# Kernel optimization log

Hardware: AMD Instinct MI355X
Metric: run time of the kernel (lower is better)

## Reference

```python
import jax, jax.numpy as jnp
import numpy as np


def setup_inputs() -> dict:
    key = jax.random.key(0)
    k1, k2, k3 = jax.random.split(key, 3)
    B, H, S, D = 4, 16, 2048, 64
    queries = jax.random.normal(k1, (B, H, S, D), dtype=jnp.float32)
    keys = jax.random.normal(k2, (B, H, S, D), dtype=jnp.float32)
    values = jax.random.normal(k3, (B, H, S, D), dtype=jnp.float32)
    return {"queries": queries, "keys": keys, "values": values, "d_k": D}


def reference(queries, keys, values, d_k):
    # scores = Q K^T / sqrt(d_k)  -> [B, H, S, S]
    scale = 1.0 / jnp.sqrt(jnp.asarray(d_k, dtype=queries.dtype))
    scores = jnp.einsum("bhqd,bhkd->bhqk", queries, keys) * scale
    weights = jax.nn.softmax(scores, axis=-1)
    # out = weights V -> [B, H, S, D]
    return jnp.einsum("bhqk,bhkd->bhqd", weights, values)
```

## Files before the change

kernel.cpp:

```cpp
#include <hip/hip_runtime.h>
#include <hip/hip_bf16.h>

typedef __attribute__((ext_vector_type(8))) short short8;
typedef __attribute__((ext_vector_type(4))) short short4v;
typedef __attribute__((ext_vector_type(16))) float f32x16;

constexpr int Sn = 2048, Dn = 64;
constexpr int KVB = 64;
constexpr int QB  = 256;
constexpr int NT  = Sn / KVB;
constexpr int KSTR = 72;
constexpr int VSTR = 68;
constexpr float QSC = 0.18033688011112042f;

struct SMemS { short K[2][KVB][KSTR]; short Vt[2][Dn][VSTR]; };
union  SMem  { SMemS s; float ep[4][32][36]; };

__device__ inline unsigned cvt_pk_bf16(float a, float b) {
  unsigned r;
  asm("v_cvt_pk_bf16_f32 %0, %1, %2" : "=v"(r) : "v"(a), "v"(b));
  return r;
}
__device__ inline short8 catw(unsigned a, unsigned b, unsigned c, unsigned d) {
  union { unsigned u[4]; short8 s; } t;
  t.u[0]=a; t.u[1]=b; t.u[2]=c; t.u[3]=d;
  return t.s;
}
__device__ inline short8 pack8(float4 a, float4 b) {
  return catw(cvt_pk_bf16(a.x,a.y), cvt_pk_bf16(a.z,a.w),
              cvt_pk_bf16(b.x,b.y), cvt_pk_bf16(b.z,b.w));
}
__device__ inline short8 cat4(short4v a, short4v b) {
  short8 r;
  r[0]=a[0]; r[1]=a[1]; r[2]=a[2]; r[3]=a[3];
  r[4]=b[0]; r[5]=b[1]; r[6]=b[2]; r[7]=b[3];
  return r;
}

__global__ __launch_bounds__(256, 2)
void attn_fwd(const float* __restrict__ Qm, const float* __restrict__ Km,
              const float* __restrict__ Vm, float* __restrict__ Om) {
  __shared__ alignas(16) SMem sm;

  const int fid = blockIdx.x + (blockIdx.y << 3);
  const int xcd = fid & 7, w = fid >> 3;
  const int qt = w & 7, bh = (xcd << 3) | (w >> 3);

  const size_t base = (size_t)bh * Sn * Dn;
  const float* Qb = Qm + base;
  const float* Kb = Km + base;
  const float* Vb = Vm + base;
  float*       Ob = Om + base;

  const int tid = threadIdx.x, wv = tid >> 6, lane = tid & 63;
  const int il = lane & 31, hi = lane >> 5;
  const int qr0 = qt * QB + wv * 64;

  short8 qf[2][4];
#pragma unroll
  for (int u = 0; u < 2; ++u)
#pragma unroll
    for (int ks = 0; ks < 4; ++ks) {
      const float4* qp = (const float4*)(Qb + (size_t)(qr0 + u*32 + il) * Dn + ks*16 + hi*8);
      float4 a = qp[0], b = qp[1];
      a.x*=QSC; a.y*=QSC; a.z*=QSC; a.w*=QSC;
      b.x*=QSC; b.y*=QSC; b.z*=QSC; b.w*=QSC;
      qf[u][ks] = pack8(a, b);
    }

  f32x16 acc[2][2];
#pragma unroll
  for (int u = 0; u < 2; ++u)
#pragma unroll
    for (int dt = 0; dt < 2; ++dt)
#pragma unroll
      for (int r = 0; r < 16; ++r) acc[u][dt][r] = 0.f;
  float lacc[2][8];
#pragma unroll
  for (int u = 0; u < 2; ++u)
#pragma unroll
    for (int r = 0; r < 8; ++r) lacc[u][r] = 0.f;

  f32x16 fz;
#pragma unroll
  for (int r = 0; r < 16; ++r) fz[r] = 0.f;

  const int krow = tid >> 2, kc = (tid & 3) * 16;
  const int vd = tid & 63, vk0 = (tid >> 6) * 8;

  auto stageK = [&](int buf, float4 a0, float4 a1, float4 a2, float4 a3) {
    *(short8*)&sm.s.K[buf][krow][kc]     = pack8(a0, a1);
    *(short8*)&sm.s.K[buf][krow][kc + 8] = pack8(a2, a3);
  };
  auto stageV = [&](int buf, const float* vv) {
#pragma unroll
    for (int c = 0; c < 2; ++c) {
      union { unsigned u[2]; short4v s; } t0, t1;
      t0.u[0] = cvt_pk_bf16(vv[c*8+0], vv[c*8+1]);
      t0.u[1] = cvt_pk_bf16(vv[c*8+2], vv[c*8+3]);
      t1.u[0] = cvt_pk_bf16(vv[c*8+4], vv[c*8+5]);
      t1.u[1] = cvt_pk_bf16(vv[c*8+6], vv[c*8+7]);
      short* p = &sm.s.Vt[buf][vd][vk0 + c*32];
      *(short4v*)p       = t0.s;
      *(short4v*)(p + 4) = t1.s;
    }
  };

  {
    const float4* kp = (const float4*)(Kb + (size_t)krow * Dn + kc);
    float4 a0 = kp[0], a1 = kp[1], a2 = kp[2], a3 = kp[3];
    float vv[16];
#pragma unroll
    for (int c = 0; c < 2; ++c)
#pragma unroll
      for (int j = 0; j < 8; ++j) vv[c*8+j] = Vb[(size_t)(vk0 + c*32 + j) * Dn + vd];
    stageK(0, a0, a1, a2, a3);
    stageV(0, vv);
  }
  __syncthreads();

  int cur = 0;
  for (int t = 0; t < NT; ++t) {
    const bool pf = (t + 1 < NT);
    float4 na0, na1, na2, na3; float nv[16];
    if (pf) {
      const int kvn = (t + 1) * KVB;
      const float4* kp = (const float4*)(Kb + (size_t)(kvn + krow) * Dn + kc);
      na0 = kp[0]; na1 = kp[1]; na2 = kp[2]; na3 = kp[3];
#pragma unroll
      for (int c = 0; c < 2; ++c)
#pragma unroll
        for (int j = 0; j < 8; ++j) nv[c*8+j] = Vb[(size_t)(kvn + vk0 + c*32 + j) * Dn + vd];
    }

    short8 kf[2][4];
#pragma unroll
    for (int h = 0; h < 2; ++h)
#pragma unroll
      for (int ks = 0; ks < 4; ++ks)
        kf[h][ks] = *(const short8*)&sm.s.K[cur][h*32 + il][ks*16 + hi*8];

    short8 vr[8];
#pragma unroll
    for (int h = 0; h < 2; ++h)
#pragma unroll
      for (int dt = 0; dt < 2; ++dt) {
        const short* vrow = &sm.s.Vt[cur][dt*32 + il][h*32];
        vr[h*4+dt*2+0] = cat4(*(const short4v*)(vrow + 4*hi),      *(const short4v*)(vrow + 8  + 4*hi));
        vr[h*4+dt*2+1] = cat4(*(const short4v*)(vrow + 16 + 4*hi), *(const short4v*)(vrow + 24 + 4*hi));
      }

    f32x16 sa[2][2];
#pragma unroll
    for (int u = 0; u < 2; ++u)
#pragma unroll
      for (int h = 0; h < 2; ++h) {
        sa[u][h] = __builtin_amdgcn_mfma_f32_32x32x16_bf16(kf[h][0], qf[u][0], fz, 0, 0, 0);
#pragma unroll
        for (int ks = 1; ks < 4; ++ks)
          sa[u][h] = __builtin_amdgcn_mfma_f32_32x32x16_bf16(kf[h][ks], qf[u][ks], sa[u][h], 0, 0, 0);
      }

    short8 pb[2][2][2];
#pragma unroll
    for (int u = 0; u < 2; ++u) {
#pragma unroll
      for (int h = 0; h < 2; ++h)
#pragma unroll
        for (int r = 0; r < 16; ++r) sa[u][h][r] = __builtin_amdgcn_exp2f(sa[u][h][r]);
      float ta[16];
#pragma unroll
      for (int r = 0; r < 16; ++r) ta[r] = sa[u][0][r] + sa[u][1][r];
#pragma unroll
      for (int r = 0; r < 8; ++r) lacc[u][r] += ta[r] + ta[r + 8];

#pragma unroll
      for (int h = 0; h < 2; ++h) {
        pb[u][h][0] = catw(cvt_pk_bf16(sa[u][h][0],  sa[u][h][1]),  cvt_pk_bf16(sa[u][h][2],  sa[u][h][3]),
                           cvt_pk_bf16(sa[u][h][4],  sa[u][h][5]),  cvt_pk_bf16(sa[u][h][6],  sa[u][h][7]));
        pb[u][h][1] = catw(cvt_pk_bf16(sa[u][h][8],  sa[u][h][9]),  cvt_pk_bf16(sa[u][h][10], sa[u][h][11]),
                           cvt_pk_bf16(sa[u][h][12], sa[u][h][13]), cvt_pk_bf16(sa[u][h][14], sa[u][h][15]));
      }
    }

    if (pf) { stageK(cur ^ 1, na0, na1, na2, na3); stageV(cur ^ 1, nv); }

#pragma unroll
    for (int h = 0; h < 2; ++h)
#pragma unroll
      for (int dt = 0; dt < 2; ++dt)
#pragma unroll
        for (int u = 0; u < 2; ++u) {
          acc[u][dt] = __builtin_amdgcn_mfma_f32_32x32x16_bf16(vr[h*4+dt*2+0], pb[u][h][0], acc[u][dt], 0, 0, 0);
          acc[u][dt] = __builtin_amdgcn_mfma_f32_32x32x16_bf16(vr[h*4+dt*2+1], pb[u][h][1], acc[u][dt], 0, 0, 0);
        }
    __syncthreads();
    cur ^= 1;
  }

  const int q2 = lane >> 1, dh = (lane & 1) * 16;
#pragma unroll
  for (int u = 0; u < 2; ++u) {
    float l0 = (lacc[u][0] + lacc[u][4]) + (lacc[u][1] + lacc[u][5]);
    float l1 = (lacc[u][2] + lacc[u][6]) + (lacc[u][3] + lacc[u][7]);
    float l  = l0 + l1;
    l += __shfl_xor(l, 32);
    const float inv = 1.0f / l;
#pragma unroll
    for (int dt = 0; dt < 2; ++dt) {
#pragma unroll
      for (int r = 0; r < 16; ++r) {
        int dcol = (r & 3) + 8 * (r >> 2) + 4 * hi;
        sm.ep[wv][il][dcol] = acc[u][dt][r] * inv;
      }
#pragma unroll
      for (int i = 0; i < 4; ++i) {
        float4 o = *(const float4*)&sm.ep[wv][q2][dh + i*4];
        *(float4*)(Ob + (size_t)(qr0 + u*32 + q2) * Dn + dt*32 + dh + i*4) = o;
      }
    }
  }
}

extern "C" void kernel_launch(void* const* d_in, const int* in_sizes, int n_in,
                              void* d_out, int out_size, void* d_ws, size_t ws_size,
                              hipStream_t stream) {
  const float* Q = (const float*)d_in[0];
  const float* K = (const float*)d_in[1];
  const float* V = (const float*)d_in[2];
  float* O = (float*)d_out;
  dim3 grid(Sn / QB, 4 * 16);
  attn_fwd<<<grid, 256, 0, stream>>>(Q, K, V, O);
}
```

Measured before the change: 85.71 us.

## Process two 64-row KV sub-tiles per barrier to halve synchronisation count

```diff
diff --git a/kernel.cpp b/kernel.cpp
--- a/kernel.cpp
+++ b/kernel.cpp
@@ -6,14 +6,13 @@
 typedef __attribute__((ext_vector_type(16))) float f32x16;
 
 constexpr int Sn = 2048, Dn = 64;
-constexpr int KVB = 64;
 constexpr int QB  = 256;
-constexpr int NT  = Sn / KVB;
+constexpr int NI  = Sn / 128;
 constexpr int KSTR = 72;
 constexpr int VSTR = 68;
 constexpr float QSC = 0.18033688011112042f;
 
-struct SMemS { short K[2][KVB][KSTR]; short Vt[2][Dn][VSTR]; };
+struct SMemS { short K[2][2][64][KSTR]; short Vt[2][2][64][VSTR]; };
 union  SMem  { SMemS s; float ep[4][32][36]; };
 
 __device__ inline unsigned cvt_pk_bf16(float a, float b) {
@@ -88,11 +87,22 @@
   const int krow = tid >> 2, kc = (tid & 3) * 16;
   const int vd = tid & 63, vk0 = (tid >> 6) * 8;
 
-  auto stageK = [&](int buf, float4 a0, float4 a1, float4 a2, float4 a3) {
-    *(short8*)&sm.s.K[buf][krow][kc]     = pack8(a0, a1);
-    *(short8*)&sm.s.K[buf][krow][kc + 8] = pack8(a2, a3);
-  };
-  auto stageV = [&](int buf, const float* vv) {
+  auto loadK = [&](int kvbase, float4* ka) {
+    const float4* kp = (const float4*)(Kb + (size_t)(kvbase + krow) * Dn + kc);
+#pragma unroll
+    for (int i = 0; i < 4; ++i) ka[i] = kp[i];
+  };
+  auto loadV = [&](int kvbase, float* vv) {
+#pragma unroll
+    for (int c = 0; c < 2; ++c)
+#pragma unroll
+      for (int j = 0; j < 8; ++j) vv[c*8+j] = Vb[(size_t)(kvbase + vk0 + c*32 + j) * Dn + vd];
+  };
+  auto stageK = [&](int buf, int sub, const float4* ka) {
+    *(short8*)&sm.s.K[buf][sub][krow][kc]     = pack8(ka[0], ka[1]);
+    *(short8*)&sm.s.K[buf][sub][krow][kc + 8] = pack8(ka[2], ka[3]);
+  };
+  auto stageV = [&](int buf, int sub, const float* vv) {
 #pragma unroll
     for (int c = 0; c < 2; ++c) {
       union { unsigned u[2]; short4v s; } t0, t1;
@@ -100,52 +110,26 @@
       t0.u[1] = cvt_pk_bf16(vv[c*8+2], vv[c*8+3]);
       t1.u[0] = cvt_pk_bf16(vv[c*8+4], vv[c*8+5]);
       t1.u[1] = cvt_pk_bf16(vv[c*8+6], vv[c*8+7]);
-      short* p = &sm.s.Vt[buf][vd][vk0 + c*32];
+      short* p = &sm.s.Vt[buf][sub][vd][vk0 + c*32];
       *(short4v*)p       = t0.s;
       *(short4v*)(p + 4) = t1.s;
     }
   };
 
-  {
-    const float4* kp = (const float4*)(Kb + (size_t)krow * Dn + kc);
-    float4 a0 = kp[0], a1 = kp[1], a2 = kp[2], a3 = kp[3];
-    float vv[16];
-#pragma unroll
-    for (int c = 0; c < 2; ++c)
-#pragma unroll
-      for (int j = 0; j < 8; ++j) vv[c*8+j] = Vb[(size_t)(vk0 + c*32 + j) * Dn + vd];
-    stageK(0, a0, a1, a2, a3);
-    stageV(0, vv);
-  }
-  __syncthreads();
-
-  int cur = 0;
-  for (int t = 0; t < NT; ++t) {
-    const bool pf = (t + 1 < NT);
-    float4 na0, na1, na2, na3; float nv[16];
-    if (pf) {
-      const int kvn = (t + 1) * KVB;
-      const float4* kp = (const float4*)(Kb + (size_t)(kvn + krow) * Dn + kc);
-      na0 = kp[0]; na1 = kp[1]; na2 = kp[2]; na3 = kp[3];
-#pragma unroll
-      for (int c = 0; c < 2; ++c)
-#pragma unroll
-        for (int j = 0; j < 8; ++j) nv[c*8+j] = Vb[(size_t)(kvn + vk0 + c*32 + j) * Dn + vd];
-    }
-
+  auto compute_sub = [&](int buf, int sub) {
     short8 kf[2][4];
 #pragma unroll
     for (int h = 0; h < 2; ++h)
 #pragma unroll
       for (int ks = 0; ks < 4; ++ks)
-        kf[h][ks] = *(const short8*)&sm.s.K[cur][h*32 + il][ks*16 + hi*8];
+        kf[h][ks] = *(const short8*)&sm.s.K[buf][sub][h*32 + il][ks*16 + hi*8];
 
     short8 vr[8];
 #pragma unroll
     for (int h = 0; h < 2; ++h)
 #pragma unroll
       for (int dt = 0; dt < 2; ++dt) {
-        const short* vrow = &sm.s.Vt[cur][dt*32 + il][h*32];
+        const short* vrow = &sm.s.Vt[buf][sub][dt*32 + il][h*32];
         vr[h*4+dt*2+0] = cat4(*(const short4v*)(vrow + 4*hi),      *(const short4v*)(vrow + 8  + 4*hi));
         vr[h*4+dt*2+1] = cat4(*(const short4v*)(vrow + 16 + 4*hi), *(const short4v*)(vrow + 24 + 4*hi));
       }
@@ -173,7 +157,6 @@
       for (int r = 0; r < 16; ++r) ta[r] = sa[u][0][r] + sa[u][1][r];
 #pragma unroll
       for (int r = 0; r < 8; ++r) lacc[u][r] += ta[r] + ta[r + 8];
-
 #pragma unroll
       for (int h = 0; h < 2; ++h) {
         pb[u][h][0] = catw(cvt_pk_bf16(sa[u][h][0],  sa[u][h][1]),  cvt_pk_bf16(sa[u][h][2],  sa[u][h][3]),
@@ -183,8 +166,6 @@
       }
     }
 
-    if (pf) { stageK(cur ^ 1, na0, na1, na2, na3); stageV(cur ^ 1, nv); }
-
 #pragma unroll
     for (int h = 0; h < 2; ++h)
 #pragma unroll
@@ -194,6 +175,34 @@
           acc[u][dt] = __builtin_amdgcn_mfma_f32_32x32x16_bf16(vr[h*4+dt*2+0], pb[u][h][0], acc[u][dt], 0, 0, 0);
           acc[u][dt] = __builtin_amdgcn_mfma_f32_32x32x16_bf16(vr[h*4+dt*2+1], pb[u][h][1], acc[u][dt], 0, 0, 0);
         }
+  };
+
+  {
+    float4 ka[4]; float vv[16];
+    loadK(0, ka);  loadV(0, vv);  stageK(0, 0, ka); stageV(0, 0, vv);
+    loadK(64, ka); loadV(64, vv); stageK(0, 1, ka); stageV(0, 1, vv);
+  }
+  __syncthreads();
+
+  int cur = 0;
+  for (int t = 0; t < NI; ++t) {
+    const bool pf = (t + 1 < NI);
+    const int kvn = (t + 1) * 128;
+    float4 ka[4]; float vv[16];
+
+    if (pf) { loadK(kvn, ka); loadV(kvn, vv); }
+
+    {
+      short8 kf[2][4];
+      (void)kf;
+    }
+    if (pf) { stageK(cur ^ 1, 0, ka); stageV(cur ^ 1, 0, vv); }
+    compute_sub(cur, 0);
+
+    if (pf) { loadK(kvn + 64, ka); loadV(kvn + 64, vv); }
+    if (pf) { stageK(cur ^ 1, 1, ka); stageV(cur ^ 1, 1, vv); }
+    compute_sub(cur, 1);
+
     __syncthreads();
     cur ^= 1;
   }
```

Result: slower. 93.70 us (+9.3%).
